# Optimization experiments

Measured on AMD Instinct MI355X. Metric: run time of the kernel, lower is better.

The kernel has to match this reference:

```python
import jax, jax.numpy as jnp
import numpy as np

R = 3.82843
FREQ = 1.0
ITERATIONS = 2

def activation_fn(x):
    # cosine squashing into [0,1], then two logistic-map iterations
    x = jnp.cos(x * FREQ) * 0.5 + 0.5
    for _ in range(ITERATIONS):
        x = R * x * (1.0 - x)
    return x

def setup_inputs() -> dict:
    key = jax.random.key(0)
    ks = jax.random.split(key, 9)
    N = 2097152
    x = jax.random.normal(ks[0], (N, 2), dtype=jnp.float32)
    def init_linear(kw, kb, fan_in, fan_out):
        # torch.nn.Linear default init: U(-1/sqrt(fan_in), 1/sqrt(fan_in))
        bound = 1.0 / np.sqrt(fan_in)
        W = jax.random.uniform(kw, (fan_out, fan_in), minval=-bound, maxval=bound, dtype=jnp.float32)
        b = jax.random.uniform(kb, (fan_out,), minval=-bound, maxval=bound, dtype=jnp.float32)
        return W, b
    W1, b1 = init_linear(ks[1], ks[2], 2, 64)
    W2, b2 = init_linear(ks[3], ks[4], 64, 64)
    W3, b3 = init_linear(ks[5], ks[6], 64, 64)
    W4, b4 = init_linear(ks[7], ks[8], 64, 1)
    return {"x": x, "W1": W1, "b1": b1, "W2": W2, "b2": b2,
            "W3": W3, "b3": b3, "W4": W4, "b4": b4}

def reference(x, W1, b1, W2, b2, W3, b3, W4, b4):
    h = activation_fn(x @ W1.T + b1)   # [N, 64]
    h = activation_fn(h @ W2.T + b2)   # [N, 64]
    h = activation_fn(h @ W3.T + b3)   # [N, 64]
    out = activation_fn(h @ W4.T + b4) # [N, 1]
    return out
```

## Files before the change

kernel.cpp:

```cpp
#include <hip/hip_runtime.h>

typedef _Float16 half8  __attribute__((ext_vector_type(8)));
typedef _Float16 half4v __attribute__((ext_vector_type(4)));
typedef _Float16 half2v __attribute__((ext_vector_type(2)));
typedef float    floatx4 __attribute__((ext_vector_type(4)));
typedef float    float2v __attribute__((ext_vector_type(2)));

static constexpr float INV2PI = 0.15915494309189535f;
static constexpr float RLOG   = 3.82843f;

static constexpr double RD = (double)RLOG;
static constexpr float ACT_A = (float)(RD*RD/4.0 - RD*RD*RD/16.0);
static constexpr float ACT_B = (float)(-RD*RD/4.0 + RD*RD*RD/8.0);
static constexpr float ACT_D = (float)(-RD*RD*RD/16.0);

__device__ __forceinline__ float act_rev(float a) {
    float c = __builtin_amdgcn_cosf(a);
    float u = c * c;
    float t = __builtin_fmaf(ACT_D, u, ACT_B);
    return __builtin_fmaf(u, t, ACT_A);
}

__device__ __forceinline__ half8 act8(floatx4 a, floatx4 b) {
    float2v c0 = { __builtin_amdgcn_cosf(a[0]), __builtin_amdgcn_cosf(a[1]) };
    float2v c1 = { __builtin_amdgcn_cosf(a[2]), __builtin_amdgcn_cosf(a[3]) };
    float2v c2 = { __builtin_amdgcn_cosf(b[0]), __builtin_amdgcn_cosf(b[1]) };
    float2v c3 = { __builtin_amdgcn_cosf(b[2]), __builtin_amdgcn_cosf(b[3]) };
    float2v u0 = c0*c0, u1 = c1*c1, u2 = c2*c2, u3 = c3*c3;
    float2v t0 = __builtin_elementwise_fma(u0, (float2v)(ACT_D), (float2v)(ACT_B));
    float2v t1 = __builtin_elementwise_fma(u1, (float2v)(ACT_D), (float2v)(ACT_B));
    float2v t2 = __builtin_elementwise_fma(u2, (float2v)(ACT_D), (float2v)(ACT_B));
    float2v t3 = __builtin_elementwise_fma(u3, (float2v)(ACT_D), (float2v)(ACT_B));
    float2v h0 = __builtin_elementwise_fma(u0, t0, (float2v)(ACT_A));
    float2v h1 = __builtin_elementwise_fma(u1, t1, (float2v)(ACT_A));
    float2v h2 = __builtin_elementwise_fma(u2, t2, (float2v)(ACT_A));
    float2v h3 = __builtin_elementwise_fma(u3, t3, (float2v)(ACT_A));
    half2v e0 = __builtin_bit_cast(half2v, __builtin_amdgcn_cvt_pkrtz(h0.x, h0.y));
    half2v e1 = __builtin_bit_cast(half2v, __builtin_amdgcn_cvt_pkrtz(h1.x, h1.y));
    half2v e2 = __builtin_bit_cast(half2v, __builtin_amdgcn_cvt_pkrtz(h2.x, h2.y));
    half2v e3 = __builtin_bit_cast(half2v, __builtin_amdgcn_cvt_pkrtz(h3.x, h3.y));
    half4v lo = __builtin_shufflevector(e0, e1, 0, 1, 2, 3);
    half4v hi = __builtin_shufflevector(e2, e3, 0, 1, 2, 3);
    return __builtin_shufflevector(lo, hi, 0, 1, 2, 3, 4, 5, 6, 7);
}

struct SMem {
    half8   w2[8][64];
    half8   w3[8][64];
    floatx4 b2[4][64];
    floatx4 b3[4][64];
};

__global__ __launch_bounds__(256, 5) void mlp_fused(
    const float* __restrict__ x,
    const float* __restrict__ W1, const float* __restrict__ b1,
    const float* __restrict__ W2, const float* __restrict__ b2,
    const float* __restrict__ W3, const float* __restrict__ b3,
    const float* __restrict__ W4, const float* __restrict__ b4,
    float* __restrict__ out, int N)
{
    __shared__ SMem sm;
    const int lane = threadIdx.x & 63;
    const int wib  = threadIdx.x >> 6;
    const int m    = lane & 15;
    const int q    = lane >> 4;
    const float s  = INV2PI;
    const floatx4 zero4 = {0.0f, 0.0f, 0.0f, 0.0f};

    half8 w1f[4];
    #pragma unroll
    for (int t = 0; t < 4; ++t) {
        half8 v = {};
        if (q == 0) {
            const int n = 16 * t + m;
            float w0 = W1[2*n] * s, w1 = W1[2*n+1] * s, bb = b1[n] * s;
            _Float16 w0h = (_Float16)w0; float w0l = w0 - (float)w0h;
            _Float16 w1h = (_Float16)w1; float w1l = w1 - (float)w1h;
            _Float16 bh  = (_Float16)bb; float bl  = bb - (float)bh;
            v[0] = w0h; v[1] = w0h; v[2] = (_Float16)w0l;
            v[3] = w1h; v[4] = w1h; v[5] = (_Float16)w1l;
            v[6] = bh;  v[7] = (_Float16)bl;
        }
        w1f[t] = v;
    }
    half8 w4f[2] = {half8{}, half8{}};
    if (m == 0) {
        #pragma unroll
        for (int c = 0; c < 2; ++c)
            #pragma unroll
            for (int j = 0; j < 8; ++j) {
                int nu = (j < 4) ? (16 * c + 4 * q + j) : (16 * (c + 2) + 4 * q + j - 4);
                w4f[c][j] = (_Float16)(W4[nu] * s);
            }
    }
    floatx4 a4init = zero4;
    if (q == 0) a4init[0] = b4[0] * s;

    if (wib == 0) {
        #pragma unroll
        for (int t = 0; t < 4; ++t) {
            const float* r2 = W2 + (16 * t + m) * 64;
            #pragma unroll
            for (int c = 0; c < 2; ++c) {
                floatx4 lo2 = *(const floatx4*)(r2 + 16 * c + 4 * q);
                floatx4 hi2 = *(const floatx4*)(r2 + 16 * (c + 2) + 4 * q);
                half8 v2;
                #pragma unroll
                for (int j = 0; j < 4; ++j) {
                    v2[j]     = (_Float16)(lo2[j] * s);
                    v2[4 + j] = (_Float16)(hi2[j] * s);
                }
                sm.w2[t * 2 + c][lane] = v2;
            }
        }
    } else if (wib == 1) {
        #pragma unroll
        for (int t = 0; t < 4; ++t) {
            const float* r3 = W3 + (16 * t + m) * 64;
            #pragma unroll
            for (int c = 0; c < 2; ++c) {
                floatx4 lo3 = *(const floatx4*)(r3 + 16 * c + 4 * q);
                floatx4 hi3 = *(const floatx4*)(r3 + 16 * (c + 2) + 4 * q);
                half8 v3;
                #pragma unroll
                for (int j = 0; j < 4; ++j) {
                    v3[j]     = (_Float16)(lo3[j] * s);
                    v3[4 + j] = (_Float16)(hi3[j] * s);
                }
                sm.w3[t * 2 + c][lane] = v3;
            }
        }
    } else if (wib == 2) {
        #pragma unroll
        for (int t = 0; t < 4; ++t) {
            sm.b2[t][lane] = *(const floatx4*)(b2 + 16 * t + 4 * q) * s;
            sm.b3[t][lane] = *(const floatx4*)(b3 + 16 * t + 4 * q) * s;
        }
    }
    __syncthreads();

    const int npairs = N >> 5;
    const int nwaves = (gridDim.x * blockDim.x) >> 6;
    const int gwave  = (int)(blockIdx.x * blockDim.x + threadIdx.x) >> 6;
    const float2* __restrict__ x2 = (const float2*)x;

    int pair = gwave;
    float2 xv0 = x2[(pair << 5) + m];
    float2 xv1 = x2[(pair << 5) + 16 + m];
    while (pair < npairs) {
        const int np = pair + nwaves;
        float2 xn0, xn1;
        if (np < npairs) {
            xn0 = x2[(np << 5) + m];
            xn1 = x2[(np << 5) + 16 + m];
        }

        half8 xa[2] = {half8{}, half8{}};
        if (q == 0) {
            float2 xs[2] = {xv0, xv1};
            #pragma unroll
            for (int u = 0; u < 2; ++u) {
                _Float16 xh = (_Float16)xs[u].x; float xl = xs[u].x - (float)xh;
                _Float16 yh = (_Float16)xs[u].y; float yl = xs[u].y - (float)yh;
                xa[u][0] = xh; xa[u][1] = (_Float16)xl; xa[u][2] = xh;
                xa[u][3] = yh; xa[u][4] = (_Float16)yl; xa[u][5] = yh;
                xa[u][6] = (_Float16)1.0f; xa[u][7] = (_Float16)1.0f;
            }
        }

        half8 B0[2], B1[2];
        #pragma unroll
        for (int u = 0; u < 2; ++u) {
            floatx4 a0 = __builtin_amdgcn_mfma_f32_16x16x32_f16(w1f[0], xa[u], zero4, 0, 0, 0);
            floatx4 a1 = __builtin_amdgcn_mfma_f32_16x16x32_f16(w1f[1], xa[u], zero4, 0, 0, 0);
            floatx4 a2 = __builtin_amdgcn_mfma_f32_16x16x32_f16(w1f[2], xa[u], zero4, 0, 0, 0);
            floatx4 a3 = __builtin_amdgcn_mfma_f32_16x16x32_f16(w1f[3], xa[u], zero4, 0, 0, 0);
            B0[u] = act8(a0, a2);
            B1[u] = act8(a1, a3);
        }

        int z2 = 0; asm volatile("" : "+v"(z2));
        const int l2i = lane + z2;
        half8 C0[2], C1[2];
        #pragma unroll
        for (int u = 0; u < 2; ++u) {
            floatx4 a0 = __builtin_amdgcn_mfma_f32_16x16x32_f16(sm.w2[0][l2i], B0[u], sm.b2[0][l2i], 0, 0, 0);
            floatx4 a1 = __builtin_amdgcn_mfma_f32_16x16x32_f16(sm.w2[2][l2i], B0[u], sm.b2[1][l2i], 0, 0, 0);
            floatx4 a2 = __builtin_amdgcn_mfma_f32_16x16x32_f16(sm.w2[4][l2i], B0[u], sm.b2[2][l2i], 0, 0, 0);
            floatx4 a3 = __builtin_amdgcn_mfma_f32_16x16x32_f16(sm.w2[6][l2i], B0[u], sm.b2[3][l2i], 0, 0, 0);
            a0 = __builtin_amdgcn_mfma_f32_16x16x32_f16(sm.w2[1][l2i], B1[u], a0, 0, 0, 0);
            a1 = __builtin_amdgcn_mfma_f32_16x16x32_f16(sm.w2[3][l2i], B1[u], a1, 0, 0, 0);
            a2 = __builtin_amdgcn_mfma_f32_16x16x32_f16(sm.w2[5][l2i], B1[u], a2, 0, 0, 0);
            a3 = __builtin_amdgcn_mfma_f32_16x16x32_f16(sm.w2[7][l2i], B1[u], a3, 0, 0, 0);
            C0[u] = act8(a0, a2);
            C1[u] = act8(a1, a3);
        }

        int z3 = 0; asm volatile("" : "+v"(z3));
        const int l3i = lane + z3;
        half8 D0[2], D1[2];
        #pragma unroll
        for (int u = 0; u < 2; ++u) {
            floatx4 a0 = __builtin_amdgcn_mfma_f32_16x16x32_f16(sm.w3[0][l3i], C0[u], sm.b3[0][l3i], 0, 0, 0);
            floatx4 a1 = __builtin_amdgcn_mfma_f32_16x16x32_f16(sm.w3[2][l3i], C0[u], sm.b3[1][l3i], 0, 0, 0);
            floatx4 a2 = __builtin_amdgcn_mfma_f32_16x16x32_f16(sm.w3[4][l3i], C0[u], sm.b3[2][l3i], 0, 0, 0);
            floatx4 a3 = __builtin_amdgcn_mfma_f32_16x16x32_f16(sm.w3[6][l3i], C0[u], sm.b3[3][l3i], 0, 0, 0);
            a0 = __builtin_amdgcn_mfma_f32_16x16x32_f16(sm.w3[1][l3i], C1[u], a0, 0, 0, 0);
            a1 = __builtin_amdgcn_mfma_f32_16x16x32_f16(sm.w3[3][l3i], C1[u], a1, 0, 0, 0);
            a2 = __builtin_amdgcn_mfma_f32_16x16x32_f16(sm.w3[5][l3i], C1[u], a2, 0, 0, 0);
            a3 = __builtin_amdgcn_mfma_f32_16x16x32_f16(sm.w3[7][l3i], C1[u], a3, 0, 0, 0);
            D0[u] = act8(a0, a2);
            D1[u] = act8(a1, a3);
        }

        floatx4 a4[2];
        #pragma unroll
        for (int u = 0; u < 2; ++u) {
            a4[u] = __builtin_amdgcn_mfma_f32_16x16x32_f16(w4f[0], D0[u], a4init, 0, 0, 0);
            a4[u] = __builtin_amdgcn_mfma_f32_16x16x32_f16(w4f[1], D1[u], a4[u], 0, 0, 0);
        }
        if (q == 0) {
            out[(pair << 5) + m]      = act_rev(a4[0][0]);
            out[(pair << 5) + 16 + m] = act_rev(a4[1][0]);
        }

        xv0 = xn0; xv1 = xn1;
        pair = np;
    }
}

extern "C" void kernel_launch(void* const* d_in, const int* in_sizes, int n_in,
                              void* d_out, int out_size, void* d_ws, size_t ws_size,
                              hipStream_t stream) {
    const float* x  = (const float*)d_in[0];
    const float* W1 = (const float*)d_in[1];
    const float* b1 = (const float*)d_in[2];
    const float* W2 = (const float*)d_in[3];
    const float* b2 = (const float*)d_in[4];
    const float* W3 = (const float*)d_in[5];
    const float* b3 = (const float*)d_in[6];
    const float* W4 = (const float*)d_in[7];
    const float* b4 = (const float*)d_in[8];
    float* out = (float*)d_out;
    const int N = out_size;

    mlp_fused<<<dim3(2560), dim3(256), 0, stream>>>(x, W1, b1, W2, b2, W3, b3, W4, b4, out, N);
}
```

Baseline: 168.7 us.

## Rewrite activation in cos(2a) form with packed fp16 polynomial; enlarge blocks

New measurement: 242.3 us. +43.6%, slower.

```diff
diff --git a/kernel.cpp b/kernel.cpp
--- a/kernel.cpp
+++ b/kernel.cpp
@@ -6,41 +6,45 @@
 typedef float    floatx4 __attribute__((ext_vector_type(4)));
 typedef float    float2v __attribute__((ext_vector_type(2)));
 
-static constexpr float INV2PI = 0.15915494309189535f;
-static constexpr float RLOG   = 3.82843f;
+static constexpr float INVPI = 0.3183098861837907f;
+static constexpr float RLOG  = 3.82843f;
 
 static constexpr double RD = (double)RLOG;
-static constexpr float ACT_A = (float)(RD*RD/4.0 - RD*RD*RD/16.0);
-static constexpr float ACT_B = (float)(-RD*RD/4.0 + RD*RD*RD/8.0);
-static constexpr float ACT_D = (float)(-RD*RD*RD/16.0);
-
-__device__ __forceinline__ float act_rev(float a) {
-    float c = __builtin_amdgcn_cosf(a);
-    float u = c * c;
-    float t = __builtin_fmaf(ACT_D, u, ACT_B);
-    return __builtin_fmaf(u, t, ACT_A);
+static constexpr double AD = RD*RD/4.0 - RD*RD*RD/16.0;
+static constexpr double BD = -RD*RD/4.0 + RD*RD*RD/8.0;
+static constexpr double DD = -RD*RD*RD/16.0;
+static constexpr float ACT_E = (float)(AD + BD/2.0 + DD/4.0);
+static constexpr float ACT_F = (float)((BD + DD)/2.0);
+static constexpr float ACT_G = (float)(DD/4.0);
+
+__device__ __forceinline__ float act_rev(float a2) {
+    float c = __builtin_amdgcn_cosf(a2);
+    float t = __builtin_fmaf(ACT_G, c, ACT_F);
+    return __builtin_fmaf(c, t, ACT_E);
 }
 
 __device__ __forceinline__ half8 act8(floatx4 a, floatx4 b) {
-    float2v c0 = { __builtin_amdgcn_cosf(a[0]), __builtin_amdgcn_cosf(a[1]) };
-    float2v c1 = { __builtin_amdgcn_cosf(a[2]), __builtin_amdgcn_cosf(a[3]) };
-    float2v c2 = { __builtin_amdgcn_cosf(b[0]), __builtin_amdgcn_cosf(b[1]) };
-    float2v c3 = { __builtin_amdgcn_cosf(b[2]), __builtin_amdgcn_cosf(b[3]) };
-    float2v u0 = c0*c0, u1 = c1*c1, u2 = c2*c2, u3 = c3*c3;
-    float2v t0 = __builtin_elementwise_fma(u0, (float2v)(ACT_D), (float2v)(ACT_B));
-    float2v t1 = __builtin_elementwise_fma(u1, (float2v)(ACT_D), (float2v)(ACT_B));
-    float2v t2 = __builtin_elementwise_fma(u2, (float2v)(ACT_D), (float2v)(ACT_B));
-    float2v t3 = __builtin_elementwise_fma(u3, (float2v)(ACT_D), (float2v)(ACT_B));
-    float2v h0 = __builtin_elementwise_fma(u0, t0, (float2v)(ACT_A));
-    float2v h1 = __builtin_elementwise_fma(u1, t1, (float2v)(ACT_A));
-    float2v h2 = __builtin_elementwise_fma(u2, t2, (float2v)(ACT_A));
-    float2v h3 = __builtin_elementwise_fma(u3, t3, (float2v)(ACT_A));
-    half2v e0 = __builtin_bit_cast(half2v, __builtin_amdgcn_cvt_pkrtz(h0.x, h0.y));
-    half2v e1 = __builtin_bit_cast(half2v, __builtin_amdgcn_cvt_pkrtz(h1.x, h1.y));
-    half2v e2 = __builtin_bit_cast(half2v, __builtin_amdgcn_cvt_pkrtz(h2.x, h2.y));
-    half2v e3 = __builtin_bit_cast(half2v, __builtin_amdgcn_cvt_pkrtz(h3.x, h3.y));
-    half4v lo = __builtin_shufflevector(e0, e1, 0, 1, 2, 3);
-    half4v hi = __builtin_shufflevector(e2, e3, 0, 1, 2, 3);
+    const half2v Gh = {(_Float16)ACT_G, (_Float16)ACT_G};
+    const half2v Fh = {(_Float16)ACT_F, (_Float16)ACT_F};
+    const half2v Eh = {(_Float16)ACT_E, (_Float16)ACT_E};
+    half2v c0 = __builtin_bit_cast(half2v, __builtin_amdgcn_cvt_pkrtz(
+                    __builtin_amdgcn_cosf(a[0]), __builtin_amdgcn_cosf(a[1])));
+    half2v c1 = __builtin_bit_cast(half2v, __builtin_amdgcn_cvt_pkrtz(
+                    __builtin_amdgcn_cosf(a[2]), __builtin_amdgcn_cosf(a[3])));
+    half2v c2 = __builtin_bit_cast(half2v, __builtin_amdgcn_cvt_pkrtz(
+                    __builtin_amdgcn_cosf(b[0]), __builtin_amdgcn_cosf(b[1])));
+    half2v c3 = __builtin_bit_cast(half2v, __builtin_amdgcn_cvt_pkrtz(
+                    __builtin_amdgcn_cosf(b[2]), __builtin_amdgcn_cosf(b[3])));
+    half2v t0 = __builtin_elementwise_fma(c0, Gh, Fh);
+    half2v t1 = __builtin_elementwise_fma(c1, Gh, Fh);
+    half2v t2 = __builtin_elementwise_fma(c2, Gh, Fh);
+    half2v t3 = __builtin_elementwise_fma(c3, Gh, Fh);
+    half2v h0 = __builtin_elementwise_fma(c0, t0, Eh);
+    half2v h1 = __builtin_elementwise_fma(c1, t1, Eh);
+    half2v h2 = __builtin_elementwise_fma(c2, t2, Eh);
+    half2v h3 = __builtin_elementwise_fma(c3, t3, Eh);
+    half4v lo = __builtin_shufflevector(h0, h1, 0, 1, 2, 3);
+    half4v hi = __builtin_shufflevector(h2, h3, 0, 1, 2, 3);
     return __builtin_shufflevector(lo, hi, 0, 1, 2, 3, 4, 5, 6, 7);
 }
 
@@ -51,7 +55,7 @@
     floatx4 b3[4][64];
 };
 
-__global__ __launch_bounds__(256, 5) void mlp_fused(
+__global__ __launch_bounds__(512, 8) void mlp_fused(
     const float* __restrict__ x,
     const float* __restrict__ W1, const float* __restrict__ b1,
     const float* __restrict__ W2, const float* __restrict__ b2,
@@ -64,7 +68,7 @@
     const int wib  = threadIdx.x >> 6;
     const int m    = lane & 15;
     const int q    = lane >> 4;
-    const float s  = INV2PI;
+    const float s  = INVPI;
     const floatx4 zero4 = {0.0f, 0.0f, 0.0f, 0.0f};
 
     half8 w1f[4];
@@ -244,5 +248,5 @@
     float* out = (float*)d_out;
     const int N = out_size;
 
-    mlp_fused<<<dim3(2560), dim3(256), 0, stream>>>(x, W1, b1, W2, b2, W3, b3, W4, b4, out, N);
-}
+    mlp_fused<<<dim3(2048), dim3(512), 0, stream>>>(x, W1, b1, W2, b2, W3, b3, W4, b4, out, N);
+}
```
